# Performance work log

Hardware: AMD Instinct MI355X
Metric: run time of the kernel (lower is better)

The kernel has to match this reference:

```python
import jax, jax.numpy as jnp
import numpy as np

IOU_THR = 0.7
SCORE_THR = 0.01
KEEP_TOPK = 300
B, N, C = 16, 2048, 80


def box_cxcywh_to_xyxy(b):
    cx, cy, w, h = b[..., 0], b[..., 1], b[..., 2], b[..., 3]
    return jnp.stack([cx - 0.5 * w, cy - 0.5 * h, cx + 0.5 * w, cy + 0.5 * h], axis=-1)


def _iou_matrix(b):
    # b: [N,4] xyxy -> [N,N] IoU
    area = (b[:, 2] - b[:, 0]) * (b[:, 3] - b[:, 1])
    lt = jnp.maximum(b[:, None, :2], b[None, :, :2])
    rb = jnp.minimum(b[:, None, 2:], b[None, :, 2:])
    wh = jnp.clip(rb - lt, 0.0)
    inter = wh[..., 0] * wh[..., 1]
    union = area[:, None] + area[None, :] - inter
    return jnp.where(union > 0, inter / union, 0.0)


def _nms_image(boxes, scores, labels):
    # boxes [N,4], scores [N], labels [N] -> padded (labels [K], boxes [K,4], scores [K])
    n = boxes.shape[0]
    s = jnp.where(scores > SCORE_THR, scores, -1.0)
    order = jnp.argsort(-s)  # descending score, thresholded-out last
    b = boxes[order]
    sc = s[order]
    lb = labels[order]
    keep0 = sc > SCORE_THR
    # batched_nms trick: offset boxes per class so different classes never overlap
    offset = lb.astype(boxes.dtype) * (jnp.max(boxes) + 1.0)
    iou = _iou_matrix(b + offset[:, None])  # [N,N]
    idxs = jnp.arange(n)

    def body(i, keep):
        sup = keep[i] & (iou[i] > IOU_THR) & (idxs > i)
        return keep & ~sup

    keep = jax.lax.fori_loop(0, n, body, keep0)
    # first KEEP_TOPK kept boxes in score order; pad invalid slots
    sel = jnp.sort(jnp.where(keep, idxs, n))[:KEEP_TOPK]
    ok = sel < n
    sel_c = jnp.minimum(sel, n - 1)
    out_b = jnp.where(ok[:, None], b[sel_c], 0.0)
    out_s = jnp.where(ok, sc[sel_c], 0.0)
    out_l = jnp.where(ok, lb[sel_c], -1)
    return out_l, out_b, out_s


def setup_inputs() -> dict:
    key = jax.random.key(0)
    k1, k2, k3 = jax.random.split(key, 3)
    pred_logits = jax.random.normal(k1, (B, N, C), dtype=jnp.float32)
    pred_boxes = jax.random.uniform(k2, (B, N, 4), dtype=jnp.float32)  # normalized cxcywh
    orig_target_sizes = 480.0 + 800.0 * jax.random.uniform(k3, (B, 2), dtype=jnp.float32)
    return {"pred_logits": pred_logits, "pred_boxes": pred_boxes,
            "orig_target_sizes": orig_target_sizes}


def reference(pred_logits, pred_boxes, orig_target_sizes):
    boxes = box_cxcywh_to_xyxy(pred_boxes)  # [B,N,4]
    scale = jnp.tile(orig_target_sizes, (1, 2))[:, None, :]  # [B,1,4] = (w,h,w,h)
    boxes = boxes * scale
    vals = jnp.max(pred_logits, axis=-1)
    labels = jnp.argmax(pred_logits, axis=-1)
    scores = jax.nn.sigmoid(vals)
    out_l, out_b, out_s = jax.vmap(_nms_image)(boxes, scores, labels)
    return out_l, out_b, out_s
```

## Files before the change

kernel.cpp:

```cpp
#include <hip/hip_runtime.h>


#define NTHREADS 1024
constexpr int Bn = 16;
constexpr int Nn = 2048;
constexpr int Cc = 80;
constexpr int Kk = 300;
constexpr int CCAP = 64;
constexpr double IOU_THR = 0.7;
constexpr double SCORE_THR = 0.01;

__device__ unsigned long long g_keys[Bn * Nn];
__device__ unsigned long long g_skeys[Bn * Nn];
__device__ unsigned char g_lab[Bn * Nn];
__device__ int g_nv[Bn];
__device__ unsigned short g_clp[Bn * Cc * CCAP];
__device__ unsigned short g_cloi[Bn * Cc * CCAP];
__device__ int g_ccnt[Bn * Cc];
__device__ unsigned int g_keepw[Bn * (Nn / 32)];

__global__ __launch_bounds__(256) void argmax_kernel(const float* __restrict__ logits)
{
    int gid = blockIdx.x * 256 + threadIdx.x;
    if (gid >= Bn * Nn) return;
    const float4* lp = (const float4*)(logits + (size_t)gid * Cc);
    float m = -__builtin_inff();
    int am = 0;
#pragma unroll
    for (int c = 0; c < Cc / 4; ++c) {
        float4 v = lp[c];
        if (v.x > m) { m = v.x; am = 4 * c + 0; }
        if (v.y > m) { m = v.y; am = 4 * c + 1; }
        if (v.z > m) { m = v.z; am = 4 * c + 2; }
        if (v.w > m) { m = v.w; am = 4 * c + 3; }
    }
    unsigned mb = __float_as_uint(m);
    unsigned asc = mb ^ ((mb & 0x80000000u) ? 0xFFFFFFFFu : 0x80000000u);
    unsigned n = (unsigned)(gid & (Nn - 1));
    g_keys[gid] = ((unsigned long long)(~asc) << 32) | n;
    g_lab[gid] = (unsigned char)am;
}

__launch_bounds__(NTHREADS, 1)
__global__ void sort_compact_kernel()
{
    __shared__ unsigned long long key[Nn];
    __shared__ unsigned char slab[Nn];
    __shared__ unsigned int hist[32 * Cc];
    __shared__ int s_nv;
    const int t = threadIdx.x;
    const int b = blockIdx.x;

    if (t == 0) s_nv = 0;
    if (t < Nn / 32) g_keepw[b * (Nn / 32) + t] = 0u;
    for (int i = t; i < 32 * Cc; i += NTHREADS) hist[i] = 0u;
    for (int p = t; p < Nn; p += NTHREADS) key[p] = g_keys[b * Nn + p];
    __syncthreads();

    int vc = 0;
    for (int p = t; p < Nn; p += NTHREADS) {
        unsigned hi = (unsigned)(key[p] >> 32);
        unsigned ascb = ~hi;
        unsigned mb = (ascb & 0x80000000u) ? (ascb ^ 0x80000000u) : ~ascb;
        float m = __uint_as_float(mb);
        double sd = 1.0 / (1.0 + exp(-(double)m));
        if (sd > SCORE_THR) vc++;
    }
    for (int off = 32; off > 0; off >>= 1) vc += __shfl_down(vc, off);
    if ((t & 63) == 0) atomicAdd(&s_nv, vc);

    for (int k = 2; k <= Nn; k <<= 1) {
        for (int j = k >> 1; j > 0; j >>= 1) {
            int i = ((t & ~(j - 1)) << 1) | (t & (j - 1));
            int p = i | j;
            bool up = ((i & k) == 0);
            unsigned long long a = key[i], c = key[p];
            if ((a > c) == up) { key[i] = c; key[p] = a; }
            __syncthreads();
        }
    }
    const int nv = s_nv;

    for (int p = t; p < Nn; p += NTHREADS) {
        int c = 127;
        if (p < nv) {
            int oi = (int)(key[p] & 0xFFFFu);
            c = (int)g_lab[b * Nn + oi];
            atomicAdd(&hist[(p >> 6) * Cc + c], 1u);
        }
        slab[p] = (unsigned char)c;
        g_skeys[b * Nn + p] = key[p];
    }
    __syncthreads();

    if (t < Cc) {
        unsigned run = 0;
        for (int ch = 0; ch < 32; ++ch) {
            unsigned v = hist[ch * Cc + t];
            hist[ch * Cc + t] = run;
            run += v;
        }
        g_ccnt[b * Cc + t] = (int)((run < CCAP) ? run : CCAP);
    }
    __syncthreads();

    const int l = t & 63;
    const unsigned long long below = (l == 0) ? 0ull : ((1ull << l) - 1ull);
#pragma unroll
    for (int half = 0; half < 2; ++half) {
        int p = half * NTHREADS + t;
        int c7 = (int)slab[p];
        unsigned long long mm = ~0ull;
#pragma unroll
        for (int bit = 0; bit < 7; ++bit) {
            unsigned long long vote = __ballot((c7 >> bit) & 1);
            mm &= ((c7 >> bit) & 1) ? vote : ~vote;
        }
        if (c7 < 127) {
            int r = (int)hist[(p >> 6) * Cc + c7] + __popcll(mm & below);
            if (r < CCAP) {
                int oi = (int)(key[p] & 0xFFFFu);
                g_clp[((size_t)b * Cc + c7) * CCAP + r] = (unsigned short)p;
                g_cloi[((size_t)b * Cc + c7) * CCAP + r] = (unsigned short)oi;
            }
        }
    }
    if (t == 0) g_nv[b] = nv;
}

__launch_bounds__(64, 8)
__global__ void pairnms_kernel(const float* __restrict__ pboxes,
                               const float* __restrict__ osize)
{
    __shared__ double lb[CCAP][5];
    const int bc = blockIdx.x;
    const int b = bc / Cc;
    const int j = threadIdx.x;
    const int cnt = g_ccnt[bc];
    if (cnt == 0) return;
    const double s0 = (double)osize[2 * b + 0];
    const double s1 = (double)osize[2 * b + 1];

    unsigned short p = 0;
    double jx1 = 0, jy1 = 0, jx2 = 0, jy2 = 0, aj = 0;
    if (j < cnt) {
        p = g_clp[(size_t)bc * CCAP + j];
        int oi = g_cloi[(size_t)bc * CCAP + j];
        const float* bp = pboxes + ((size_t)b * Nn + oi) * 4;
        double cx = (double)bp[0], cy = (double)bp[1];
        double w  = (double)bp[2], h  = (double)bp[3];
        jx1 = (cx - 0.5 * w) * s0; jy1 = (cy - 0.5 * h) * s1;
        jx2 = (cx + 0.5 * w) * s0; jy2 = (cy + 0.5 * h) * s1;
        aj = (jx2 - jx1) * (jy2 - jy1);
        lb[j][0] = jx1; lb[j][1] = jy1; lb[j][2] = jx2; lb[j][3] = jy2; lb[j][4] = aj;
    }
    __syncthreads();

    unsigned long long mymask = 0ull;
    if (j < cnt) {
        for (int i = 0; i < j; ++i) {
            double lt0 = fmax(lb[i][0], jx1), lt1 = fmax(lb[i][1], jy1);
            double rb0 = fmin(lb[i][2], jx2), rb1 = fmin(lb[i][3], jy2);
            double w0 = fmax(rb0 - lt0, 0.0), w1 = fmax(rb1 - lt1, 0.0);
            double inter = w0 * w1;
            double uni = lb[i][4] + aj - inter;
            if (uni > 0.0 && inter > IOU_THR * uni) mymask |= 1ull << i;
        }
    }

    unsigned long long K = 0ull;
    for (int r = 0; r < cnt; ++r) {
        unsigned long long mr = __shfl(mymask, r);
        if ((mr & K) == 0ull) K |= 1ull << r;
    }
    if (j < cnt && ((K >> j) & 1ull))
        atomicOr(&g_keepw[b * (Nn / 32) + (p >> 5)], 1u << (p & 31));
}

#define FT 512
__launch_bounds__(FT, 1)
__global__ void finalize_kernel(const float* __restrict__ pboxes,
                                const float* __restrict__ osize,
                                float* __restrict__ out)
{
    __shared__ unsigned int kw[Nn / 32];
    __shared__ int kpre[Nn / 32];
    __shared__ int out_posS[Kk];
    __shared__ int s_kept;
    const int t = threadIdx.x;
    const int b = blockIdx.x;
    const double s0 = (double)osize[2 * b + 0];
    const double s1 = (double)osize[2 * b + 1];

    if (t < Nn / 32) kw[t] = g_keepw[b * (Nn / 32) + t];
    __syncthreads();
    if (t < 64) {
        unsigned w = kw[t];
        int pc = __popc(w);
        int inc = pc;
        for (int off = 1; off < 64; off <<= 1) {
            int v = __shfl_up(inc, off);
            if (t >= off) inc += v;
        }
        kpre[t] = inc - pc;
        if (t == 63) s_kept = (inc < Kk) ? inc : Kk;
    }
    __syncthreads();
    for (int p = t; p < Nn; p += FT) {
        if ((kw[p >> 5] >> (p & 31)) & 1u) {
            int rank = kpre[p >> 5] + __popc(kw[p >> 5] & ((1u << (p & 31)) - 1u));
            if (rank < Kk) out_posS[rank] = p;
        }
    }
    __syncthreads();

    const int kept = s_kept;
    const int base_b = Bn * Kk;
    const int base_s = Bn * Kk * 5;
    for (int r = t; r < Kk; r += FT) {
        float lf = -1.0f, b0 = 0.f, b1 = 0.f, b2 = 0.f, b3 = 0.f, sf = 0.f;
        if (r < kept) {
            int p = out_posS[r];
            unsigned long long kk = g_skeys[b * Nn + p];
            unsigned oi = (unsigned)(kk & 0xFFFFu);
            lf = (float)g_lab[b * Nn + oi];
            unsigned hi = (unsigned)(kk >> 32);
            unsigned ascb = ~hi;
            unsigned mb = (ascb & 0x80000000u) ? (ascb ^ 0x80000000u) : ~ascb;
            float m = __uint_as_float(mb);
            sf = (float)(1.0 / (1.0 + exp(-(double)m)));
            const float* bp = pboxes + ((size_t)b * Nn + oi) * 4;
            double cx = (double)bp[0], cy = (double)bp[1];
            double w  = (double)bp[2], h  = (double)bp[3];
            b0 = (float)((cx - 0.5 * w) * s0);
            b1 = (float)((cy - 0.5 * h) * s1);
            b2 = (float)((cx + 0.5 * w) * s0);
            b3 = (float)((cy + 0.5 * h) * s1);
        }
        out[b * Kk + r] = lf;
        float* ob = out + base_b + (size_t)(b * Kk + r) * 4;
        ob[0] = b0; ob[1] = b1; ob[2] = b2; ob[3] = b3;
        out[base_s + b * Kk + r] = sf;
    }
}

extern "C" void kernel_launch(void* const* d_in, const int* in_sizes, int n_in,
                              void* d_out, int out_size, void* d_ws, size_t ws_size,
                              hipStream_t stream)
{
    const float* logits = (const float*)d_in[0];
    const float* pboxes = (const float*)d_in[1];
    const float* osize  = (const float*)d_in[2];
    float* out = (float*)d_out;
    argmax_kernel<<<(Bn * Nn + 255) / 256, 256, 0, stream>>>(logits);
    sort_compact_kernel<<<Bn, NTHREADS, 0, stream>>>();
    pairnms_kernel<<<Bn * Cc, 64, 0, stream>>>(pboxes, osize);
    finalize_kernel<<<Bn, FT, 0, stream>>>(pboxes, osize, out);
}
```

Before: 41.37 us.

## Register/shuffle bitonic sort and move per-class compaction into pairnms blocks

New measurement: 49.85 us. 1.2x slower.

```diff
diff --git a/kernel.cpp b/kernel.cpp
--- a/kernel.cpp
+++ b/kernel.cpp
@@ -13,10 +13,7 @@
 __device__ unsigned long long g_keys[Bn * Nn];
 __device__ unsigned long long g_skeys[Bn * Nn];
 __device__ unsigned char g_lab[Bn * Nn];
-__device__ int g_nv[Bn];
-__device__ unsigned short g_clp[Bn * Cc * CCAP];
-__device__ unsigned short g_cloi[Bn * Cc * CCAP];
-__device__ int g_ccnt[Bn * Cc];
+__device__ unsigned char g_slab[Bn * Nn];
 __device__ unsigned int g_keepw[Bn * (Nn / 32)];
 
 __global__ __launch_bounds__(256) void argmax_kernel(const float* __restrict__ logits)
@@ -41,116 +38,126 @@
     g_lab[gid] = (unsigned char)am;
 }
 
+__device__ __forceinline__ void cx(unsigned long long& a, unsigned long long p, bool takeMin)
+{
+    bool aless = a < p;
+    a = (takeMin == aless) ? a : p;
+}
+
 __launch_bounds__(NTHREADS, 1)
-__global__ void sort_compact_kernel()
-{
-    __shared__ unsigned long long key[Nn];
-    __shared__ unsigned char slab[Nn];
-    __shared__ unsigned int hist[32 * Cc];
+__global__ void sort_kernel()
+{
+    __shared__ unsigned long long buf[2][Nn];
     __shared__ int s_nv;
     const int t = threadIdx.x;
     const int b = blockIdx.x;
+    const size_t base = (size_t)b * Nn;
 
     if (t == 0) s_nv = 0;
     if (t < Nn / 32) g_keepw[b * (Nn / 32) + t] = 0u;
-    for (int i = t; i < 32 * Cc; i += NTHREADS) hist[i] = 0u;
-    for (int p = t; p < Nn; p += NTHREADS) key[p] = g_keys[b * Nn + p];
-    __syncthreads();
-
-    int vc = 0;
-    for (int p = t; p < Nn; p += NTHREADS) {
-        unsigned hi = (unsigned)(key[p] >> 32);
-        unsigned ascb = ~hi;
-        unsigned mb = (ascb & 0x80000000u) ? (ascb ^ 0x80000000u) : ~ascb;
-        float m = __uint_as_float(mb);
-        double sd = 1.0 / (1.0 + exp(-(double)m));
-        if (sd > SCORE_THR) vc++;
-    }
-    for (int off = 32; off > 0; off >>= 1) vc += __shfl_down(vc, off);
-    if ((t & 63) == 0) atomicAdd(&s_nv, vc);
-
+
+    unsigned long long v0 = g_keys[base + t];
+    unsigned long long v1 = g_keys[base + t + 1024];
+
+    {
+        int vc = 0;
+#pragma unroll
+        for (int e = 0; e < 2; ++e) {
+            unsigned hi = (unsigned)((e ? v1 : v0) >> 32);
+            unsigned ascb = ~hi;
+            unsigned mb = (ascb & 0x80000000u) ? (ascb ^ 0x80000000u) : ~ascb;
+            float m = __uint_as_float(mb);
+            double sd = 1.0 / (1.0 + exp(-(double)m));
+            if (sd > SCORE_THR) vc++;
+        }
+        for (int off = 32; off > 0; off >>= 1) vc += __shfl_down(vc, off);
+        if ((t & 63) == 0) atomicAdd(&s_nv, vc);
+    }
+
+    int cur = 0;
     for (int k = 2; k <= Nn; k <<= 1) {
         for (int j = k >> 1; j > 0; j >>= 1) {
-            int i = ((t & ~(j - 1)) << 1) | (t & (j - 1));
-            int p = i | j;
-            bool up = ((i & k) == 0);
-            unsigned long long a = key[i], c = key[p];
-            if ((a > c) == up) { key[i] = c; key[p] = a; }
-            __syncthreads();
-        }
-    }
+            if (j >= 1024) {
+                unsigned long long mn = (v0 < v1) ? v0 : v1;
+                unsigned long long mx = (v0 < v1) ? v1 : v0;
+                v0 = mn; v1 = mx;
+            } else if (j >= 64) {
+                buf[cur][t] = v0;
+                buf[cur][t + 1024] = v1;
+                __syncthreads();
+                unsigned long long p0 = buf[cur][t ^ j];
+                unsigned long long p1 = buf[cur][(t ^ j) + 1024];
+                bool lower = ((t & j) == 0);
+                cx(v0, p0, lower == ((t & k) == 0));
+                cx(v1, p1, lower == (((t + 1024) & k) == 0));
+                cur ^= 1;
+            } else {
+                unsigned long long p0 = __shfl_xor(v0, j);
+                unsigned long long p1 = __shfl_xor(v1, j);
+                bool lower = ((t & j) == 0);
+                cx(v0, p0, lower == ((t & k) == 0));
+                cx(v1, p1, lower == (((t + 1024) & k) == 0));
+            }
+        }
+    }
+    __syncthreads();
     const int nv = s_nv;
 
-    for (int p = t; p < Nn; p += NTHREADS) {
-        int c = 127;
-        if (p < nv) {
-            int oi = (int)(key[p] & 0xFFFFu);
-            c = (int)g_lab[b * Nn + oi];
-            atomicAdd(&hist[(p >> 6) * Cc + c], 1u);
-        }
-        slab[p] = (unsigned char)c;
-        g_skeys[b * Nn + p] = key[p];
-    }
-    __syncthreads();
-
-    if (t < Cc) {
-        unsigned run = 0;
-        for (int ch = 0; ch < 32; ++ch) {
-            unsigned v = hist[ch * Cc + t];
-            hist[ch * Cc + t] = run;
-            run += v;
-        }
-        g_ccnt[b * Cc + t] = (int)((run < CCAP) ? run : CCAP);
-    }
-    __syncthreads();
-
-    const int l = t & 63;
-    const unsigned long long below = (l == 0) ? 0ull : ((1ull << l) - 1ull);
-#pragma unroll
-    for (int half = 0; half < 2; ++half) {
-        int p = half * NTHREADS + t;
-        int c7 = (int)slab[p];
-        unsigned long long mm = ~0ull;
-#pragma unroll
-        for (int bit = 0; bit < 7; ++bit) {
-            unsigned long long vote = __ballot((c7 >> bit) & 1);
-            mm &= ((c7 >> bit) & 1) ? vote : ~vote;
-        }
-        if (c7 < 127) {
-            int r = (int)hist[(p >> 6) * Cc + c7] + __popcll(mm & below);
-            if (r < CCAP) {
-                int oi = (int)(key[p] & 0xFFFFu);
-                g_clp[((size_t)b * Cc + c7) * CCAP + r] = (unsigned short)p;
-                g_cloi[((size_t)b * Cc + c7) * CCAP + r] = (unsigned short)oi;
-            }
-        }
-    }
-    if (t == 0) g_nv[b] = nv;
+    {
+        int oi0 = (int)(v0 & 0xFFFFu);
+        int oi1 = (int)(v1 & 0xFFFFu);
+        g_skeys[base + t] = v0;
+        g_skeys[base + t + 1024] = v1;
+        g_slab[base + t] = (t < nv) ? g_lab[base + oi0] : (unsigned char)127;
+        g_slab[base + t + 1024] = (t + 1024 < nv) ? g_lab[base + oi1] : (unsigned char)127;
+    }
 }
 
 __launch_bounds__(64, 8)
 __global__ void pairnms_kernel(const float* __restrict__ pboxes,
                                const float* __restrict__ osize)
 {
+    __shared__ unsigned int item[CCAP];
     __shared__ double lb[CCAP][5];
     const int bc = blockIdx.x;
     const int b = bc / Cc;
-    const int j = threadIdx.x;
-    const int cnt = g_ccnt[bc];
+    const int c = bc - b * Cc;
+    const int l = threadIdx.x;
+    const unsigned char* sl = g_slab + (size_t)b * Nn;
+    const unsigned long long below = (l == 0) ? 0ull : ((1ull << l) - 1ull);
+
+    int cnt = 0;
+    for (int p0 = 0; p0 < Nn && cnt < CCAP; p0 += 64) {
+        int p = p0 + l;
+        bool match = ((int)sl[p] == c);
+        unsigned long long mk = __ballot(match);
+        if (match) {
+            int r = cnt + __popcll(mk & below);
+            if (r < CCAP) {
+                int oi = (int)(g_skeys[(size_t)b * Nn + p] & 0xFFFFu);
+                item[r] = ((unsigned)oi << 16) | (unsigned)p;
+            }
+        }
+        cnt += __popcll(mk);
+    }
+    if (cnt > CCAP) cnt = CCAP;
     if (cnt == 0) return;
+    __syncthreads();
+
     const double s0 = (double)osize[2 * b + 0];
     const double s1 = (double)osize[2 * b + 1];
-
-    unsigned short p = 0;
+    const int j = l;
+    unsigned pos = 0;
     double jx1 = 0, jy1 = 0, jx2 = 0, jy2 = 0, aj = 0;
     if (j < cnt) {
-        p = g_clp[(size_t)bc * CCAP + j];
-        int oi = g_cloi[(size_t)bc * CCAP + j];
+        unsigned it = item[j];
+        pos = it & 0xFFFFu;
+        int oi = (int)(it >> 16);
         const float* bp = pboxes + ((size_t)b * Nn + oi) * 4;
-        double cx = (double)bp[0], cy = (double)bp[1];
+        double cx_ = (double)bp[0], cy_ = (double)bp[1];
         double w  = (double)bp[2], h  = (double)bp[3];
-        jx1 = (cx - 0.5 * w) * s0; jy1 = (cy - 0.5 * h) * s1;
-        jx2 = (cx + 0.5 * w) * s0; jy2 = (cy + 0.5 * h) * s1;
+        jx1 = (cx_ - 0.5 * w) * s0; jy1 = (cy_ - 0.5 * h) * s1;
+        jx2 = (cx_ + 0.5 * w) * s0; jy2 = (cy_ + 0.5 * h) * s1;
         aj = (jx2 - jx1) * (jy2 - jy1);
         lb[j][0] = jx1; lb[j][1] = jy1; lb[j][2] = jx2; lb[j][3] = jy2; lb[j][4] = aj;
     }
@@ -174,7 +181,7 @@
         if ((mr & K) == 0ull) K |= 1ull << r;
     }
     if (j < cnt && ((K >> j) & 1ull))
-        atomicOr(&g_keepw[b * (Nn / 32) + (p >> 5)], 1u << (p & 31));
+        atomicOr(&g_keepw[b * (Nn / 32) + (pos >> 5)], 1u << (pos & 31));
 }
 
 #define FT 512
@@ -221,9 +228,9 @@
         float lf = -1.0f, b0 = 0.f, b1 = 0.f, b2 = 0.f, b3 = 0.f, sf = 0.f;
         if (r < kept) {
             int p = out_posS[r];
-            unsigned long long kk = g_skeys[b * Nn + p];
+            unsigned long long kk = g_skeys[(size_t)b * Nn + p];
             unsigned oi = (unsigned)(kk & 0xFFFFu);
-            lf = (float)g_lab[b * Nn + oi];
+            lf = (float)g_lab[(size_t)b * Nn + oi];
             unsigned hi = (unsigned)(kk >> 32);
             unsigned ascb = ~hi;
             unsigned mb = (ascb & 0x80000000u) ? (ascb ^ 0x80000000u) : ~ascb;
@@ -253,7 +260,7 @@
     const float* osize  = (const float*)d_in[2];
     float* out = (float*)d_out;
     argmax_kernel<<<(Bn * Nn + 255) / 256, 256, 0, stream>>>(logits);
-    sort_compact_kernel<<<Bn, NTHREADS, 0, stream>>>();
+    sort_kernel<<<Bn, NTHREADS, 0, stream>>>();
     pairnms_kernel<<<Bn * Cc, 64, 0, stream>>>(pboxes, osize);
     finalize_kernel<<<Bn, FT, 0, stream>>>(pboxes, osize, out);
 }
```

## Rewrite bitonic sort with register keys, wave shuffles and double-buffered LDS

Applied to the files above, without the earlier changes.

Measured after the change: 42.33 us. 2.3% more time.

```diff
diff --git a/kernel.cpp b/kernel.cpp
--- a/kernel.cpp
+++ b/kernel.cpp
@@ -13,7 +13,6 @@
 __device__ unsigned long long g_keys[Bn * Nn];
 __device__ unsigned long long g_skeys[Bn * Nn];
 __device__ unsigned char g_lab[Bn * Nn];
-__device__ int g_nv[Bn];
 __device__ unsigned short g_clp[Bn * Cc * CCAP];
 __device__ unsigned short g_cloi[Bn * Cc * CCAP];
 __device__ int g_ccnt[Bn * Cc];
@@ -41,56 +40,80 @@
     g_lab[gid] = (unsigned char)am;
 }
 
+__device__ __forceinline__ void cx(unsigned long long& a, unsigned long long p, bool takeMin)
+{
+    bool aless = a < p;
+    a = (takeMin == aless) ? a : p;
+}
+
 __launch_bounds__(NTHREADS, 1)
 __global__ void sort_compact_kernel()
 {
-    __shared__ unsigned long long key[Nn];
-    __shared__ unsigned char slab[Nn];
+    __shared__ unsigned long long dbuf[2][Nn];
     __shared__ unsigned int hist[32 * Cc];
     __shared__ int s_nv;
     const int t = threadIdx.x;
     const int b = blockIdx.x;
+    const size_t base = (size_t)b * Nn;
 
     if (t == 0) s_nv = 0;
     if (t < Nn / 32) g_keepw[b * (Nn / 32) + t] = 0u;
     for (int i = t; i < 32 * Cc; i += NTHREADS) hist[i] = 0u;
-    for (int p = t; p < Nn; p += NTHREADS) key[p] = g_keys[b * Nn + p];
-    __syncthreads();
-
-    int vc = 0;
-    for (int p = t; p < Nn; p += NTHREADS) {
-        unsigned hi = (unsigned)(key[p] >> 32);
-        unsigned ascb = ~hi;
-        unsigned mb = (ascb & 0x80000000u) ? (ascb ^ 0x80000000u) : ~ascb;
-        float m = __uint_as_float(mb);
-        double sd = 1.0 / (1.0 + exp(-(double)m));
-        if (sd > SCORE_THR) vc++;
-    }
-    for (int off = 32; off > 0; off >>= 1) vc += __shfl_down(vc, off);
-    if ((t & 63) == 0) atomicAdd(&s_nv, vc);
-
+
+    unsigned long long v0 = g_keys[base + t];
+    unsigned long long v1 = g_keys[base + t + 1024];
+
+    {
+        int vc = 0;
+#pragma unroll
+        for (int e = 0; e < 2; ++e) {
+            unsigned hi = (unsigned)((e ? v1 : v0) >> 32);
+            unsigned ascb = ~hi;
+            unsigned mb = (ascb & 0x80000000u) ? (ascb ^ 0x80000000u) : ~ascb;
+            float m = __uint_as_float(mb);
+            double sd = 1.0 / (1.0 + exp(-(double)m));
+            if (sd > SCORE_THR) vc++;
+        }
+        for (int off = 32; off > 0; off >>= 1) vc += __shfl_down(vc, off);
+        if ((t & 63) == 0) atomicAdd(&s_nv, vc);
+    }
+
+    int cur = 0;
     for (int k = 2; k <= Nn; k <<= 1) {
         for (int j = k >> 1; j > 0; j >>= 1) {
-            int i = ((t & ~(j - 1)) << 1) | (t & (j - 1));
-            int p = i | j;
-            bool up = ((i & k) == 0);
-            unsigned long long a = key[i], c = key[p];
-            if ((a > c) == up) { key[i] = c; key[p] = a; }
-            __syncthreads();
+            if (j >= 1024) {
+                unsigned long long mn = (v0 < v1) ? v0 : v1;
+                unsigned long long mx = (v0 < v1) ? v1 : v0;
+                v0 = mn; v1 = mx;
+            } else if (j >= 64) {
+                dbuf[cur][t] = v0;
+                dbuf[cur][t + 1024] = v1;
+                __syncthreads();
+                unsigned long long p0 = dbuf[cur][t ^ j];
+                unsigned long long p1 = dbuf[cur][(t ^ j) + 1024];
+                bool lower = ((t & j) == 0);
+                cx(v0, p0, lower == ((t & k) == 0));
+                cx(v1, p1, lower == (((t + 1024) & k) == 0));
+                cur ^= 1;
+            } else {
+                unsigned long long p0 = __shfl_xor(v0, j);
+                unsigned long long p1 = __shfl_xor(v1, j);
+                bool lower = ((t & j) == 0);
+                cx(v0, p0, lower == ((t & k) == 0));
+                cx(v1, p1, lower == (((t + 1024) & k) == 0));
+            }
         }
     }
     const int nv = s_nv;
 
-    for (int p = t; p < Nn; p += NTHREADS) {
-        int c = 127;
-        if (p < nv) {
-            int oi = (int)(key[p] & 0xFFFFu);
-            c = (int)g_lab[b * Nn + oi];
-            atomicAdd(&hist[(p >> 6) * Cc + c], 1u);
-        }
-        slab[p] = (unsigned char)c;
-        g_skeys[b * Nn + p] = key[p];
-    }
+    const int oi0 = (int)(v0 & 0xFFFFu);
+    const int oi1 = (int)(v1 & 0xFFFFu);
+    const int c0 = (t < nv) ? (int)g_lab[base + oi0] : 127;
+    const int c1 = (t + 1024 < nv) ? (int)g_lab[base + oi1] : 127;
+    if (c0 < 127) atomicAdd(&hist[(t >> 6) * Cc + c0], 1u);
+    if (c1 < 127) atomicAdd(&hist[((t + 1024) >> 6) * Cc + c1], 1u);
+    g_skeys[base + t] = v0;
+    g_skeys[base + t + 1024] = v1;
     __syncthreads();
 
     if (t < Cc) {
@@ -107,9 +130,10 @@
     const int l = t & 63;
     const unsigned long long below = (l == 0) ? 0ull : ((1ull << l) - 1ull);
 #pragma unroll
-    for (int half = 0; half < 2; ++half) {
-        int p = half * NTHREADS + t;
-        int c7 = (int)slab[p];
+    for (int e = 0; e < 2; ++e) {
+        const int p = e ? (t + 1024) : t;
+        const int c7 = e ? c1 : c0;
+        const int oi = e ? oi1 : oi0;
         unsigned long long mm = ~0ull;
 #pragma unroll
         for (int bit = 0; bit < 7; ++bit) {
@@ -119,13 +143,11 @@
         if (c7 < 127) {
             int r = (int)hist[(p >> 6) * Cc + c7] + __popcll(mm & below);
             if (r < CCAP) {
-                int oi = (int)(key[p] & 0xFFFFu);
                 g_clp[((size_t)b * Cc + c7) * CCAP + r] = (unsigned short)p;
                 g_cloi[((size_t)b * Cc + c7) * CCAP + r] = (unsigned short)oi;
             }
         }
     }
-    if (t == 0) g_nv[b] = nv;
 }
 
 __launch_bounds__(64, 8)
@@ -221,9 +243,9 @@
         float lf = -1.0f, b0 = 0.f, b1 = 0.f, b2 = 0.f, b3 = 0.f, sf = 0.f;
         if (r < kept) {
             int p = out_posS[r];
-            unsigned long long kk = g_skeys[b * Nn + p];
+            unsigned long long kk = g_skeys[(size_t)b * Nn + p];
             unsigned oi = (unsigned)(kk & 0xFFFFu);
-            lf = (float)g_lab[b * Nn + oi];
+            lf = (float)g_lab[(size_t)b * Nn + oi];
             unsigned hi = (unsigned)(kk >> 32);
             unsigned ascb = ~hi;
             unsigned mb = (ascb & 0x80000000u) ? (ascb ^ 0x80000000u) : ~ascb;
```
